# Kernel tuning notes

Measured on AMD Instinct MI355X. Metric: run time of the kernel, lower is better.

## Reference

```python
import jax, jax.numpy as jnp
import numpy as np

SCALE = 1.0 / np.sqrt(512.0).astype(np.float32)  # attention() hardcodes d_k=512


def setup_inputs() -> dict:
    key = jax.random.key(0)
    ks = jax.random.split(key, 9)
    B, S, D = 4, 2048, 512
    mk = lambda k, shape: jax.random.normal(k, shape, dtype=jnp.float32) * 0.05
    return {
        "q": mk(ks[0], (B, S, D)),
        "k": mk(ks[1], (B, S, D)),
        "v": mk(ks[2], (B, S, D)),
        "WQ_w": mk(ks[3], (D, D)),
        "WQ_b": mk(ks[4], (D,)),
        "WK_w": mk(ks[5], (D, D)),
        "WK_b": mk(ks[6], (D,)),
        "WV_w": mk(ks[7], (D, D)),
        "WV_b": mk(ks[8], (D,)),
    }


def reference(q, k, v, WQ_w, WQ_b, WK_w, WK_b, WV_w, WV_b):
    # torch nn.Linear: y = x @ W.T + b
    qp = q @ WQ_w.T + WQ_b  # [B,S,dk]
    kp = k @ WK_w.T + WK_b  # [B,S,dk]
    vp = v @ WV_w.T + WV_b  # [B,S,dv]
    qk = jnp.einsum("bqd,bkd->bqk", qp, kp) * SCALE  # [B,Sq,Sk]
    S = qk.shape[1]
    tril = jnp.tril(jnp.ones((S, S), dtype=qk.dtype))  # multiplicative causal mask
    qk = qk * tril
    # NOTE: original applies softmax over dim=1 (the query axis), faithfully kept.
    attn = jax.nn.softmax(qk, axis=1)
    out = jnp.einsum("bqk,bkd->bqd", attn, vp)  # [B,Sq,dv]
    return out
```

## Files before the change

kernel.cpp:

```cpp
#include <hip/hip_runtime.h>
#include <hip/hip_bf16.h>


#define S_LEN 2048
#define D_DIM 512
#define SCALE_F 0.044194173824159216f

typedef __attribute__((ext_vector_type(8))) short s8v;
typedef __attribute__((ext_vector_type(4))) short s4v;
typedef __attribute__((ext_vector_type(4))) float f4v;

enum { EPI_BIAS = 0, EPI_BIAS_T = 1, EPI_SCORES = 2 };

#define SBAR()    __builtin_amdgcn_s_barrier()
#define SCHEDB()  __builtin_amdgcn_sched_barrier(0)
#define WAITV(n)  asm volatile("s_waitcnt vmcnt(" #n ")")
#define WAITL0()  asm volatile("s_waitcnt lgkmcnt(0)")

__device__ __forceinline__ short f2bf_s(float f) {
  union { __hip_bfloat16 b; short s; } u; u.b = __float2bfloat16(f); return u.s;
}
__device__ __forceinline__ float bf2f_s(short h) {
  union { short s; __hip_bfloat16 b; } u; u.s = h; return __bfloat162float(u.b);
}

__device__ __forceinline__ void glds16(const short* g, short* l) {
  __builtin_amdgcn_global_load_lds((const __attribute__((address_space(1))) void*)g,
                                   (__attribute__((address_space(3))) void*)l, 16, 0, 0);
}

__device__ __forceinline__ unsigned lds_addr(const short* p) {
  return (unsigned)(unsigned long long)(const __attribute__((address_space(3))) short*)p;
}

__device__ __forceinline__ s8v dsr128(unsigned a) {
  s8v r;
  asm volatile("ds_read_b128 %0, %1" : "=&v"(r) : "v"(a));
  return r;
}

template <int EPI>
__device__ __forceinline__ void gemm_core(
    const short* __restrict__ A, const short* __restrict__ B,
    short* __restrict__ C, const float* __restrict__ bias,
    short* SMEM, int N, int K, size_t sCz, int m0, int n0, int bz,
    float* __restrict__ Z)
{
  const int tid  = threadIdx.x;
  const int w    = tid >> 6;
  const int lane = tid & 63;
  const int quad = lane >> 4;
  const int l16  = lane & 15;
  const int wm   = (w >> 1) * 64;
  const int wn   = (w & 1) * 64;

  const int strow = tid >> 3;
  const int gl = ((tid & 7) ^ (strow & 7)) * 8;

  f4v acc[4][4];
#pragma unroll
  for (int i = 0; i < 4; ++i)
#pragma unroll
    for (int j = 0; j < 4; ++j)
#pragma unroll
      for (int r = 0; r < 4; ++r) acc[i][j][r] = 0.0f;

  const short* Ag = A + (size_t)(m0 + strow) * K + gl;
  const short* Bg = B + (size_t)(n0 + strow) * K + gl;
  const size_t pstr = (size_t)32 * K;
  const int t8 = tid * 8;
  const int swq = l16 & 7;

  const unsigned base = lds_addr(SMEM);
  unsigned aoff[4], boff[4];
#pragma unroll
  for (int ii = 0; ii < 4; ++ii)
    aoff[ii] = base + (unsigned)((wm + ii * 16 + l16) * 128 + ((quad ^ swq) * 16));
#pragma unroll
  for (int j = 0; j < 4; ++j)
    boff[j] = base + 16384u + (unsigned)((wn + j * 16 + l16) * 128 + ((quad ^ swq) * 16));

  const int niter = K >> 6;

#pragma unroll
  for (int p = 0; p < 4; ++p) glds16(Ag + p * pstr, SMEM + t8 + p * 2048);
#pragma unroll
  for (int p = 0; p < 4; ++p) glds16(Bg + p * pstr, SMEM + 8192 + t8 + p * 2048);

  for (int i = 0; i < niter; ++i) {
    const int c = i & 1;
    if (i + 1 < niter) {
      const int k1 = (i + 1) << 6;
      short* dA = SMEM + (1 - c) * 16384 + t8;
#pragma unroll
      for (int p = 0; p < 4; ++p) glds16(Ag + k1 + p * pstr, dA + p * 2048);
#pragma unroll
      for (int p = 0; p < 4; ++p) glds16(Bg + k1 + p * pstr, dA + 8192 + p * 2048);
      SCHEDB();
      WAITV(8);
    } else {
      WAITV(0);
    }
    SBAR();
    SCHEDB();

    const unsigned cofs = (unsigned)(c << 15);
#pragma unroll
    for (int kk = 0; kk < 2; ++kk) {
      const unsigned kx = (unsigned)(kk << 6);
      s8v af[4], bf[4];
#pragma unroll
      for (int ii = 0; ii < 4; ++ii) af[ii] = dsr128((aoff[ii] ^ kx) + cofs);
#pragma unroll
      for (int j = 0; j < 4; ++j)   bf[j]  = dsr128((boff[j] ^ kx) + cofs);
      WAITL0();
      SCHEDB();
      __builtin_amdgcn_s_setprio(1);
#pragma unroll
      for (int ii = 0; ii < 4; ++ii)
#pragma unroll
        for (int j = 0; j < 4; ++j)
          acc[ii][j] = __builtin_amdgcn_mfma_f32_16x16x32_bf16(af[ii], bf[j], acc[ii][j], 0, 0, 0);
      __builtin_amdgcn_s_setprio(0);
    }
    SBAR();
  }

  float bv[4];
  if (EPI == EPI_BIAS || EPI == EPI_BIAS_T) {
#pragma unroll
    for (int j = 0; j < 4; ++j) bv[j] = bias[n0 + wn + j * 16 + l16];
  }

  if (EPI == EPI_BIAS_T) {
#pragma unroll
    for (int i = 0; i < 4; ++i) {
#pragma unroll
      for (int j = 0; j < 4; ++j) {
        const int gn  = n0 + wn + j * 16 + l16;
        const int gmb = m0 + wm + i * 16 + quad * 4;
        const int bb = gmb >> 11, ssb = gmb & (S_LEN - 1);
        s4v o;
#pragma unroll
        for (int r = 0; r < 4; ++r) o[r] = f2bf_s(acc[i][j][r] + bv[j]);
        *(s4v*)&C[((size_t)bb * D_DIM + gn) * S_LEN + ssb] = o;
      }
    }
    return;
  }

  short* TB = SMEM;
  const int wbase = w * 2176;
  float csum[4] = {0.f, 0.f, 0.f, 0.f};

#pragma unroll
  for (int ph = 0; ph < 2; ++ph) {
    __syncthreads();
#pragma unroll
    for (int ii = 0; ii < 2; ++ii) {
      const int i = ph * 2 + ii;
#pragma unroll
      for (int j = 0; j < 4; ++j) {
        const int gn = n0 + wn + j * 16 + l16;
#pragma unroll
        for (int r = 0; r < 4; ++r) {
          short o;
          if (EPI == EPI_SCORES) {
            const int gm = m0 + wm + i * 16 + quad * 4 + r;
            const float f = (gm >= gn) ? (__expf(acc[i][j][r] * SCALE_F) - 1.0f) : 0.0f;
            csum[j] += f;
            o = f2bf_s(f);
          } else {
            o = f2bf_s(acc[i][j][r] + bv[j]);
          }
          TB[wbase + (ii * 16 + quad * 4 + r) * 68 + j * 16 + l16] = o;
        }
      }
    }
    __syncthreads();
#pragma unroll
    for (int p = 0; p < 4; ++p) {
      const int row = p * 8 + (lane >> 3);
      const int cg  = lane & 7;
      const s8v vv = *(const s8v*)&TB[wbase + row * 68 + cg * 8];
      const int gm = m0 + wm + ph * 32 + row;
      const int gn = n0 + wn + cg * 8;
      *(s8v*)&C[sCz + (size_t)gm * N + gn] = vv;
    }
  }

  if (EPI == EPI_SCORES) {
#pragma unroll
    for (int j = 0; j < 4; ++j) {
      float cs = csum[j];
      cs += __shfl_xor(cs, 16, 64);
      cs += __shfl_xor(cs, 32, 64);
      if (quad == 0) atomicAdd(&Z[(bz << 11) + n0 + wn + j * 16 + l16], cs);
    }
  }
}

__global__ __launch_bounds__(256, 2) void proj_qk(
    const short* __restrict__ a0, const short* __restrict__ a1,
    const short* __restrict__ b0, const short* __restrict__ b1,
    short* __restrict__ c0, short* __restrict__ c1,
    const float* __restrict__ x0, const float* __restrict__ x1)
{
  __shared__ __align__(16) short SMEM[32768];
  const int bid = blockIdx.x;
  const int bsw = (bid & 7) * 64 + (bid >> 3);
  const int z   = bsw >> 8;
  const int rem = bsw & 255;
  const int m0  = (rem >> 2) * 128;
  const int n0  = (rem & 3) * 128;
  const short* A = z ? a1 : a0;
  const short* B = z ? b1 : b0;
  short*       C = z ? c1 : c0;
  const float* bias = z ? x1 : x0;
  gemm_core<EPI_BIAS>(A, B, C, bias, SMEM, D_DIM, D_DIM, 0, m0, n0, 0, nullptr);
}

__global__ __launch_bounds__(256, 2) void scores_projv(
    const short* __restrict__ qp, const short* __restrict__ kp, short* __restrict__ F,
    float* __restrict__ Z,
    const short* __restrict__ vb, const short* __restrict__ Wvb,
    short* __restrict__ vpT, const float* __restrict__ xv)
{
  __shared__ __align__(16) short SMEM[32768];
  const int bid = blockIdx.x;
  if (bid < 544) {
    const int bsw = (bid & 7) * 68 + (bid >> 3);
    const int bz  = bsw / 136;
    const int t   = bsw - bz * 136;
    int ti = (int)((sqrtf(8.0f * t + 1.0f) - 1.0f) * 0.5f);
    while ((ti + 1) * (ti + 2) / 2 <= t) ++ti;
    while (ti * (ti + 1) / 2 > t) --ti;
    const int tj = t - ti * (ti + 1) / 2;
    gemm_core<EPI_SCORES>(qp + (size_t)bz * S_LEN * D_DIM, kp + (size_t)bz * S_LEN * D_DIM,
                          F, nullptr, SMEM, S_LEN, D_DIM,
                          (size_t)bz * S_LEN * S_LEN, ti * 128, tj * 128, bz, Z);
  } else {
    const int h   = bid - 544;
    const int hsw = (h & 7) * 32 + (h >> 3);
    const int m0  = (hsw >> 2) * 128;
    const int n0  = (hsw & 3) * 128;
    gemm_core<EPI_BIAS_T>(vb, Wvb, vpT, xv, SMEM, D_DIM, D_DIM, 0, m0, n0, 0, nullptr);
  }
}

__global__ __launch_bounds__(256, 2) void gemm_outF(
    const short* __restrict__ F, const short* __restrict__ vpT,
    const float* __restrict__ Tv, float* __restrict__ out)
{
  __shared__ __align__(16) short SMEM[36864];

  const int tid  = threadIdx.x;
  const int h    = blockIdx.x;
  const int n0   = (h & 3) * 128;
  const int bz   = (h >> 2) & 3;
  const int zs   = h >> 4;
  const int mi   = (zs < 16) ? (31 - zs) : (zs - 16);
  const int m0   = mi * 64;

  const short* A = F   + (size_t)bz * S_LEN * S_LEN;
  const short* B = vpT + (size_t)bz * D_DIM * S_LEN;

  const int w    = tid >> 6;
  const int lane = tid & 63;
  const int quad = lane >> 4;
  const int l16  = lane & 15;
  const int wm   = (w >> 1) * 32;
  const int wn   = (w & 1) * 64;

  const int strow = tid >> 3;
  const int gl = ((tid & 7) ^ (strow & 7)) * 8;

  f4v acc[2][4];
#pragma unroll
  for (int i = 0; i < 2; ++i)
#pragma unroll
    for (int j = 0; j < 4; ++j)
#pragma unroll
      for (int r = 0; r < 4; ++r) acc[i][j][r] = 0.0f;

  const short* Ag = A + (size_t)(m0 + strow) * S_LEN + gl;
  const short* Bg = B + (size_t)(n0 + strow) * S_LEN + gl;
  const size_t pstr = (size_t)32 * S_LEN;
  const int t8 = tid * 8;
  const int swq = l16 & 7;

  const unsigned base = lds_addr(SMEM);
  unsigned aoff[2], boff[4];
#pragma unroll
  for (int ii = 0; ii < 2; ++ii)
    aoff[ii] = base + (unsigned)((wm + ii * 16 + l16) * 128 + ((quad ^ swq) * 16));
#pragma unroll
  for (int j = 0; j < 4; ++j)
    boff[j] = base + 8192u + (unsigned)((wn + j * 16 + l16) * 128 + ((quad ^ swq) * 16));

  const int niter = mi + 1;

#pragma unroll
  for (int pre = 0; pre < 2; ++pre) {
    short* dst = SMEM + pre * 12288 + t8;
    const int k0 = pre << 6;
#pragma unroll
    for (int p = 0; p < 2; ++p) glds16(Ag + k0 + p * pstr, dst + p * 2048);
#pragma unroll
    for (int p = 0; p < 4; ++p) glds16(Bg + k0 + p * pstr, dst + 4096 + p * 2048);
  }

  int cbuf = 0;
  for (int i = 0; i < niter; ++i) {
    if (i + 1 < niter) { WAITV(6); } else { WAITV(0); }
    SBAR();
    SCHEDB();

    if (i + 2 < niter) {
      int nb = cbuf + 2; if (nb >= 3) nb -= 3;
      const int k2 = (i + 2) << 6;
      short* dst = SMEM + nb * 12288 + t8;
#pragma unroll
      for (int p = 0; p < 2; ++p) glds16(Ag + k2 + p * pstr, dst + p * 2048);
#pragma unroll
      for (int p = 0; p < 4; ++p) glds16(Bg + k2 + p * pstr, dst + 4096 + p * 2048);
      SCHEDB();
    }

    const unsigned cofs = (unsigned)(cbuf * 24576);
    cbuf = (cbuf == 2) ? 0 : cbuf + 1;
#pragma unroll
    for (int kk = 0; kk < 2; ++kk) {
      const unsigned kx = (unsigned)(kk << 6);
      s8v af[2], bf[4];
#pragma unroll
      for (int ii = 0; ii < 2; ++ii) af[ii] = dsr128((aoff[ii] ^ kx) + cofs);
#pragma unroll
      for (int j = 0; j < 4; ++j)   bf[j]  = dsr128((boff[j] ^ kx) + cofs);
      WAITL0();
      SCHEDB();
      __builtin_amdgcn_s_setprio(1);
#pragma unroll
      for (int ii = 0; ii < 2; ++ii)
#pragma unroll
        for (int j = 0; j < 4; ++j)
          acc[ii][j] = __builtin_amdgcn_mfma_f32_16x16x32_bf16(af[ii], bf[j], acc[ii][j], 0, 0, 0);
      __builtin_amdgcn_s_setprio(0);
    }
  }

  float* Cf = out + (size_t)bz * S_LEN * D_DIM;
#pragma unroll
  for (int i = 0; i < 2; ++i) {
#pragma unroll
    for (int j = 0; j < 4; ++j) {
      const int gn = n0 + wn + j * 16 + l16;
      const float tvn = Tv[(bz << 9) + gn];
#pragma unroll
      for (int r = 0; r < 4; ++r) {
        const int gm = m0 + wm + i * 16 + quad * 4 + r;
        Cf[(size_t)gm * D_DIM + gn] = acc[i][j][r] + tvn;
      }
    }
  }
}

__global__ __launch_bounds__(256) void cvt_all(
    const float* __restrict__ q, const float* __restrict__ k, const float* __restrict__ v,
    const float* __restrict__ wq, const float* __restrict__ wk, const float* __restrict__ wv,
    short* __restrict__ qb, short* __restrict__ kb, short* __restrict__ vb,
    short* __restrict__ Wqb, short* __restrict__ Wkb, short* __restrict__ Wvb,
    float* __restrict__ ZF)
{
  const int y = blockIdx.y;
  const float* s; short* d; int i;
  if (blockIdx.x < 2048) {
    s = (y == 0) ? q : (y == 1) ? k : v;
    d = (y == 0) ? qb : (y == 1) ? kb : vb;
    i = (blockIdx.x * 256 + threadIdx.x) * 8;
    if (y == 0) {
      const int gid = blockIdx.x * 256 + threadIdx.x;
      if (gid < 8192) ZF[gid] = 0.0f;
    }
  } else {
    s = (y == 0) ? wq : (y == 1) ? wk : wv;
    d = (y == 0) ? Wqb : (y == 1) ? Wkb : Wvb;
    i = ((int)(blockIdx.x - 2048) * 256 + threadIdx.x) * 8;
  }
  const float4 f0 = *(const float4*)(s + i);
  const float4 f1 = *(const float4*)(s + i + 4);
  s8v o;
  o[0] = f2bf_s(f0.x); o[1] = f2bf_s(f0.y); o[2] = f2bf_s(f0.z); o[3] = f2bf_s(f0.w);
  o[4] = f2bf_s(f1.x); o[5] = f2bf_s(f1.y); o[6] = f2bf_s(f1.z); o[7] = f2bf_s(f1.w);
  *(s8v*)(d + i) = o;
}

__global__ __launch_bounds__(256) void scale_vpt_T(
    short* __restrict__ vpT, const float* __restrict__ ZF, float* __restrict__ Tv)
{
  __shared__ float red[4];
  const int b = blockIdx.y, d = blockIdx.x, tid = threadIdx.x;
  const size_t rowbase = ((size_t)(b * D_DIM + d)) * S_LEN;
  const float* zf = ZF + (b << 11);
  const int k0 = tid * 8;

  s8v v = *(s8v*)&vpT[rowbase + k0];
  float s = 0.0f;
#pragma unroll
  for (int i = 0; i < 8; ++i) {
    const float w = bf2f_s(v[i]) / (2048.0f + zf[k0 + i]);
    s += w;
    v[i] = f2bf_s(w);
  }
  *(s8v*)&vpT[rowbase + k0] = v;

#pragma unroll
  for (int off = 32; off >= 1; off >>= 1) s += __shfl_xor(s, off, 64);
  if ((tid & 63) == 0) red[tid >> 6] = s;
  __syncthreads();
  if (tid == 0) Tv[(b << 9) + d] = red[0] + red[1] + red[2] + red[3];
}

extern "C" void kernel_launch(void* const* d_in, const int* in_sizes, int n_in,
                              void* d_out, int out_size, void* d_ws, size_t ws_size,
                              hipStream_t stream) {
  const float* q   = (const float*)d_in[0];
  const float* k   = (const float*)d_in[1];
  const float* v   = (const float*)d_in[2];
  const float* WQw = (const float*)d_in[3];
  const float* WQb = (const float*)d_in[4];
  const float* WKw = (const float*)d_in[5];
  const float* WKb = (const float*)d_in[6];
  const float* WVw = (const float*)d_in[7];
  const float* WVb = (const float*)d_in[8];

  char* ws = (char*)d_ws;
  short* F   = (short*)(ws);
  short* qb  = (short*)(ws);
  short* kb  = qb + 4194304;
  short* Wqb = (short*)(ws + 25165824);
  short* Wkb = Wqb + 262144;
  short* qp  = (short*)(ws + 33554432);
  short* kp  = (short*)(ws + 41943040);
  short* vpT = (short*)(ws + 50331648);
  float* ZF  = (float*)(ws + 58720256);
  float* Tv  = (float*)(ws + 58753024);
  short* vb  = (short*)d_out;
  short* Wvb = (short*)d_out + 4194304;

  const dim3 blk(256);

  cvt_all<<<dim3(2176, 3), blk, 0, stream>>>(
      q, k, v, WQw, WKw, WVw, qb, kb, vb, Wqb, Wkb, Wvb, ZF);

  proj_qk<<<dim3(512), blk, 0, stream>>>(qb, kb, Wqb, Wkb, qp, kp, WQb, WKb);

  scores_projv<<<dim3(800), blk, 0, stream>>>(qp, kp, F, ZF, vb, Wvb, vpT, WVb);

  scale_vpt_T<<<dim3(512, 4), blk, 0, stream>>>(vpT, ZF, Tv);

  gemm_outF<<<dim3(512), blk, 0, stream>>>(F, vpT, Tv, (float*)d_out);
}
```

Measured before the change: 164.4 us.

## Use 256x256 GEMM tiles with 512 threads and fold V projection into projection kernel

Replaces the 128x128, 256-thread GEMM core with a 256x256, 512-thread core that stages 64-wide K slices into 128KB of dynamic LDS. Each wave now computes a 128x64 sub-tile, with B fragments reused across four A phases. The Q, K and V projections run in one 192-block launch, and the causal score GEMM uses 144 triangular 256x256 tiles. The aim is more operand reuse per LDS load and fewer launches and blocks, at the cost of far fewer blocks than CUs, one block per CU because of the LDS size, and more wasted work on diagonal tiles.

```diff
diff --git a/kernel.cpp b/kernel.cpp
--- a/kernel.cpp
+++ b/kernel.cpp
@@ -40,62 +40,61 @@
 }
 
 template <int EPI>
-__device__ __forceinline__ void gemm_core(
+__device__ __forceinline__ void gemm256_core(
     const short* __restrict__ A, const short* __restrict__ B,
     short* __restrict__ C, const float* __restrict__ bias,
-    short* SMEM, int N, int K, size_t sCz, int m0, int n0, int bz,
-    float* __restrict__ Z)
+    short* SMEM, int N, size_t sCz, int m0, int n0, float* __restrict__ Z)
 {
   const int tid  = threadIdx.x;
   const int w    = tid >> 6;
   const int lane = tid & 63;
   const int quad = lane >> 4;
   const int l16  = lane & 15;
-  const int wm   = (w >> 1) * 64;
-  const int wn   = (w & 1) * 64;
+  const int wr   = w >> 2;
+  const int wc   = w & 3;
 
   const int strow = tid >> 3;
   const int gl = ((tid & 7) ^ (strow & 7)) * 8;
-
-  f4v acc[4][4];
-#pragma unroll
-  for (int i = 0; i < 4; ++i)
-#pragma unroll
-    for (int j = 0; j < 4; ++j)
-#pragma unroll
-      for (int r = 0; r < 4; ++r) acc[i][j][r] = 0.0f;
-
-  const short* Ag = A + (size_t)(m0 + strow) * K + gl;
-  const short* Bg = B + (size_t)(n0 + strow) * K + gl;
-  const size_t pstr = (size_t)32 * K;
   const int t8 = tid * 8;
   const int swq = l16 & 7;
 
+  f4v acc[8][4];
+#pragma unroll
+  for (int i = 0; i < 8; ++i)
+#pragma unroll
+    for (int j = 0; j < 4; ++j)
+#pragma unroll
+      for (int r = 0; r < 4; ++r) acc[i][j][r] = 0.0f;
+
+  const short* Ag = A + (size_t)(m0 + strow) * 512 + gl;
+  const short* Bg = B + (size_t)(n0 + strow) * 512 + gl;
+  const size_t pstr = (size_t)64 * 512;
+
   const unsigned base = lds_addr(SMEM);
-  unsigned aoff[4], boff[4];
-#pragma unroll
-  for (int ii = 0; ii < 4; ++ii)
-    aoff[ii] = base + (unsigned)((wm + ii * 16 + l16) * 128 + ((quad ^ swq) * 16));
-#pragma unroll
-  for (int j = 0; j < 4; ++j)
-    boff[j] = base + 16384u + (unsigned)((wn + j * 16 + l16) * 128 + ((quad ^ swq) * 16));
-
-  const int niter = K >> 6;
-
-#pragma unroll
-  for (int p = 0; p < 4; ++p) glds16(Ag + p * pstr, SMEM + t8 + p * 2048);
-#pragma unroll
-  for (int p = 0; p < 4; ++p) glds16(Bg + p * pstr, SMEM + 8192 + t8 + p * 2048);
-
-  for (int i = 0; i < niter; ++i) {
-    const int c = i & 1;
-    if (i + 1 < niter) {
-      const int k1 = (i + 1) << 6;
-      short* dA = SMEM + (1 - c) * 16384 + t8;
-#pragma unroll
-      for (int p = 0; p < 4; ++p) glds16(Ag + k1 + p * pstr, dA + p * 2048);
-#pragma unroll
-      for (int p = 0; p < 4; ++p) glds16(Bg + k1 + p * pstr, dA + 8192 + p * 2048);
+  unsigned aoff[8], boff[4];
+#pragma unroll
+  for (int mf = 0; mf < 8; ++mf)
+    aoff[mf] = base + (unsigned)((wr * 128 + mf * 16 + l16) * 128 + ((quad ^ swq) * 16));
+#pragma unroll
+  for (int nf = 0; nf < 4; ++nf)
+    boff[nf] = base + 32768u + (unsigned)((wc * 64 + nf * 16 + l16) * 128 + ((quad ^ swq) * 16));
+
+#define STG256(kt, b)                                                          \
+  {                                                                            \
+    short* dst_ = SMEM + (b) * 32768 + t8;                                     \
+    const int ko_ = (kt) << 6;                                                 \
+    _Pragma("unroll")                                                          \
+    for (int p = 0; p < 4; ++p) glds16(Ag + ko_ + p * pstr, dst_ + p * 4096);  \
+    _Pragma("unroll")                                                          \
+    for (int p = 0; p < 4; ++p) glds16(Bg + ko_ + p * pstr, dst_ + 16384 + p * 4096); \
+  }
+
+  STG256(0, 0);
+
+  for (int t = 0; t < 8; ++t) {
+    const int c = t & 1;
+    if (t < 7) {
+      STG256(t + 1, 1 - c);
       SCHEDB();
       WAITV(8);
     } else {
@@ -104,45 +103,58 @@
     SBAR();
     SCHEDB();
 
-    const unsigned cofs = (unsigned)(c << 15);
-#pragma unroll
-    for (int kk = 0; kk < 2; ++kk) {
-      const unsigned kx = (unsigned)(kk << 6);
-      s8v af[4], bf[4];
-#pragma unroll
-      for (int ii = 0; ii < 4; ++ii) af[ii] = dsr128((aoff[ii] ^ kx) + cofs);
-#pragma unroll
-      for (int j = 0; j < 4; ++j)   bf[j]  = dsr128((boff[j] ^ kx) + cofs);
+    const unsigned cofs = (unsigned)(c << 16);
+
+    s8v bf[2][4];
+#pragma unroll
+    for (int kk = 0; kk < 2; ++kk)
+#pragma unroll
+      for (int nf = 0; nf < 4; ++nf)
+        bf[kk][nf] = dsr128((boff[nf] ^ (unsigned)(kk << 6)) + cofs);
+
+#pragma unroll
+    for (int ph = 0; ph < 4; ++ph) {
+      s8v af[2][2];
+#pragma unroll
+      for (int mi = 0; mi < 2; ++mi)
+#pragma unroll
+        for (int kk = 0; kk < 2; ++kk)
+          af[mi][kk] = dsr128((aoff[ph * 2 + mi] ^ (unsigned)(kk << 6)) + cofs);
       WAITL0();
       SCHEDB();
       __builtin_amdgcn_s_setprio(1);
 #pragma unroll
-      for (int ii = 0; ii < 4; ++ii)
-#pragma unroll
-        for (int j = 0; j < 4; ++j)
-          acc[ii][j] = __builtin_amdgcn_mfma_f32_16x16x32_bf16(af[ii], bf[j], acc[ii][j], 0, 0, 0);
+      for (int mi = 0; mi < 2; ++mi)
+#pragma unroll
+        for (int kk = 0; kk < 2; ++kk)
+#pragma unroll
+          for (int nf = 0; nf < 4; ++nf)
+            acc[ph * 2 + mi][nf] =
+                __builtin_amdgcn_mfma_f32_16x16x32_bf16(af[mi][kk], bf[kk][nf],
+                                                        acc[ph * 2 + mi][nf], 0, 0, 0);
       __builtin_amdgcn_s_setprio(0);
-    }
-    SBAR();
-  }
+      SBAR();
+    }
+  }
+#undef STG256
 
   float bv[4];
   if (EPI == EPI_BIAS || EPI == EPI_BIAS_T) {
 #pragma unroll
-    for (int j = 0; j < 4; ++j) bv[j] = bias[n0 + wn + j * 16 + l16];
+    for (int nf = 0; nf < 4; ++nf) bv[nf] = bias[n0 + wc * 64 + nf * 16 + l16];
   }
 
   if (EPI == EPI_BIAS_T) {
 #pragma unroll
-    for (int i = 0; i < 4; ++i) {
-#pragma unroll
-      for (int j = 0; j < 4; ++j) {
-        const int gn  = n0 + wn + j * 16 + l16;
-        const int gmb = m0 + wm + i * 16 + quad * 4;
+    for (int mf = 0; mf < 8; ++mf) {
+#pragma unroll
+      for (int nf = 0; nf < 4; ++nf) {
+        const int gn  = n0 + wc * 64 + nf * 16 + l16;
+        const int gmb = m0 + wr * 128 + mf * 16 + quad * 4;
         const int bb = gmb >> 11, ssb = gmb & (S_LEN - 1);
         s4v o;
 #pragma unroll
-        for (int r = 0; r < 4; ++r) o[r] = f2bf_s(acc[i][j][r] + bv[j]);
+        for (int r = 0; r < 4; ++r) o[r] = f2bf_s(acc[mf][nf][r] + bv[nf]);
         *(s4v*)&C[((size_t)bb * D_DIM + gn) * S_LEN + ssb] = o;
       }
     }
@@ -154,26 +166,26 @@
   float csum[4] = {0.f, 0.f, 0.f, 0.f};
 
 #pragma unroll
-  for (int ph = 0; ph < 2; ++ph) {
+  for (int ph = 0; ph < 4; ++ph) {
     __syncthreads();
 #pragma unroll
     for (int ii = 0; ii < 2; ++ii) {
-      const int i = ph * 2 + ii;
-#pragma unroll
-      for (int j = 0; j < 4; ++j) {
-        const int gn = n0 + wn + j * 16 + l16;
+      const int mf = ph * 2 + ii;
+#pragma unroll
+      for (int nf = 0; nf < 4; ++nf) {
+        const int gn = n0 + wc * 64 + nf * 16 + l16;
 #pragma unroll
         for (int r = 0; r < 4; ++r) {
           short o;
           if (EPI == EPI_SCORES) {
-            const int gm = m0 + wm + i * 16 + quad * 4 + r;
-            const float f = (gm >= gn) ? (__expf(acc[i][j][r] * SCALE_F) - 1.0f) : 0.0f;
-            csum[j] += f;
+            const int gm = m0 + wr * 128 + mf * 16 + quad * 4 + r;
+            const float f = (gm >= gn) ? (__expf(acc[mf][nf][r] * SCALE_F) - 1.0f) : 0.0f;
+            csum[nf] += f;
             o = f2bf_s(f);
           } else {
-            o = f2bf_s(acc[i][j][r] + bv[j]);
+            o = f2bf_s(acc[mf][nf][r] + bv[nf]);
           }
-          TB[wbase + (ii * 16 + quad * 4 + r) * 68 + j * 16 + l16] = o;
+          TB[wbase + (ii * 16 + quad * 4 + r) * 68 + nf * 16 + l16] = o;
         }
       }
     }
@@ -183,69 +195,63 @@
       const int row = p * 8 + (lane >> 3);
       const int cg  = lane & 7;
       const s8v vv = *(const s8v*)&TB[wbase + row * 68 + cg * 8];
-      const int gm = m0 + wm + ph * 32 + row;
-      const int gn = n0 + wn + cg * 8;
+      const int gm = m0 + wr * 128 + ph * 32 + row;
+      const int gn = n0 + wc * 64 + cg * 8;
       *(s8v*)&C[sCz + (size_t)gm * N + gn] = vv;
     }
   }
 
   if (EPI == EPI_SCORES) {
 #pragma unroll
-    for (int j = 0; j < 4; ++j) {
-      float cs = csum[j];
+    for (int nf = 0; nf < 4; ++nf) {
+      float cs = csum[nf];
       cs += __shfl_xor(cs, 16, 64);
       cs += __shfl_xor(cs, 32, 64);
-      if (quad == 0) atomicAdd(&Z[(bz << 11) + n0 + wn + j * 16 + l16], cs);
-    }
-  }
-}
-
-__global__ __launch_bounds__(256, 2) void proj_qk(
-    const short* __restrict__ a0, const short* __restrict__ a1,
-    const short* __restrict__ b0, const short* __restrict__ b1,
-    short* __restrict__ c0, short* __restrict__ c1,
-    const float* __restrict__ x0, const float* __restrict__ x1)
-{
-  __shared__ __align__(16) short SMEM[32768];
+      if (quad == 0) atomicAdd(&Z[n0 + wc * 64 + nf * 16 + l16], cs);
+    }
+  }
+}
+
+__global__ __launch_bounds__(512, 2) void proj256(
+    const short* __restrict__ qb, const short* __restrict__ kb, const short* __restrict__ vb,
+    const short* __restrict__ Wqb, const short* __restrict__ Wkb, const short* __restrict__ Wvb,
+    short* __restrict__ qp, short* __restrict__ kp, short* __restrict__ vpT,
+    const float* __restrict__ xq, const float* __restrict__ xk, const float* __restrict__ xv)
+{
+  extern __shared__ short SMEM[];
   const int bid = blockIdx.x;
-  const int bsw = (bid & 7) * 64 + (bid >> 3);
-  const int z   = bsw >> 8;
-  const int rem = bsw & 255;
-  const int m0  = (rem >> 2) * 128;
-  const int n0  = (rem & 3) * 128;
-  const short* A = z ? a1 : a0;
-  const short* B = z ? b1 : b0;
-  short*       C = z ? c1 : c0;
-  const float* bias = z ? x1 : x0;
-  gemm_core<EPI_BIAS>(A, B, C, bias, SMEM, D_DIM, D_DIM, 0, m0, n0, 0, nullptr);
-}
-
-__global__ __launch_bounds__(256, 2) void scores_projv(
+  const int bsw = (bid & 7) * 24 + (bid >> 3);
+  const int z   = bsw >> 6;
+  const int rem = bsw & 63;
+  const int m0  = (rem >> 1) * 256;
+  const int n0  = (rem & 1) * 256;
+  const short* A = (z == 0) ? qb : (z == 1) ? kb : vb;
+  const short* B = (z == 0) ? Wqb : (z == 1) ? Wkb : Wvb;
+  short*       C = (z == 0) ? qp : (z == 1) ? kp : vpT;
+  const float* bias = (z == 0) ? xq : (z == 1) ? xk : xv;
+  if (z == 2)
+    gemm256_core<EPI_BIAS_T>(A, B, C, bias, SMEM, D_DIM, 0, m0, n0, nullptr);
+  else
+    gemm256_core<EPI_BIAS>(A, B, C, bias, SMEM, D_DIM, 0, m0, n0, nullptr);
+}
+
+__global__ __launch_bounds__(512, 2) void scores256(
     const short* __restrict__ qp, const short* __restrict__ kp, short* __restrict__ F,
-    float* __restrict__ Z,
-    const short* __restrict__ vb, const short* __restrict__ Wvb,
-    short* __restrict__ vpT, const float* __restrict__ xv)
-{
-  __shared__ __align__(16) short SMEM[32768];
+    float* __restrict__ Z)
+{
+  extern __shared__ short SMEM[];
   const int bid = blockIdx.x;
-  if (bid < 544) {
-    const int bsw = (bid & 7) * 68 + (bid >> 3);
-    const int bz  = bsw / 136;
-    const int t   = bsw - bz * 136;
-    int ti = (int)((sqrtf(8.0f * t + 1.0f) - 1.0f) * 0.5f);
-    while ((ti + 1) * (ti + 2) / 2 <= t) ++ti;
-    while (ti * (ti + 1) / 2 > t) --ti;
-    const int tj = t - ti * (ti + 1) / 2;
-    gemm_core<EPI_SCORES>(qp + (size_t)bz * S_LEN * D_DIM, kp + (size_t)bz * S_LEN * D_DIM,
-                          F, nullptr, SMEM, S_LEN, D_DIM,
-                          (size_t)bz * S_LEN * S_LEN, ti * 128, tj * 128, bz, Z);
-  } else {
-    const int h   = bid - 544;
-    const int hsw = (h & 7) * 32 + (h >> 3);
-    const int m0  = (hsw >> 2) * 128;
-    const int n0  = (hsw & 3) * 128;
-    gemm_core<EPI_BIAS_T>(vb, Wvb, vpT, xv, SMEM, D_DIM, D_DIM, 0, m0, n0, 0, nullptr);
-  }
+  const int bsw = (bid & 7) * 18 + (bid >> 3);
+  const int bz  = bsw / 36;
+  const int t   = bsw - bz * 36;
+  int ti = (int)((sqrtf(8.0f * t + 1.0f) - 1.0f) * 0.5f);
+  while ((ti + 1) * (ti + 2) / 2 <= t) ++ti;
+  while (ti * (ti + 1) / 2 > t) --ti;
+  const int tj = t - ti * (ti + 1) / 2;
+  gemm256_core<EPI_SCORES>(qp + (size_t)bz * S_LEN * D_DIM, kp + (size_t)bz * S_LEN * D_DIM,
+                           F, nullptr, SMEM, S_LEN,
+                           (size_t)bz * S_LEN * S_LEN, ti * 256, tj * 256,
+                           Z + (bz << 11));
 }
 
 __global__ __launch_bounds__(256, 2) void gemm_outF(
@@ -438,24 +444,34 @@
   short* F   = (short*)(ws);
   short* qb  = (short*)(ws);
   short* kb  = qb + 4194304;
+  short* vb  = qb + 8388608;
   short* Wqb = (short*)(ws + 25165824);
   short* Wkb = Wqb + 262144;
+  short* Wvb = Wqb + 524288;
   short* qp  = (short*)(ws + 33554432);
   short* kp  = (short*)(ws + 41943040);
   short* vpT = (short*)(ws + 50331648);
   float* ZF  = (float*)(ws + 58720256);
   float* Tv  = (float*)(ws + 58753024);
-  short* vb  = (short*)d_out;
-  short* Wvb = (short*)d_out + 4194304;
+
+  static bool attr_done = false;
+  if (!attr_done) {
+    (void)hipFuncSetAttribute((const void*)proj256,
+                              hipFuncAttributeMaxDynamicSharedMemorySize, 131072);
+    (void)hipFuncSetAttribute((const void*)scores256,
+                              hipFuncAttributeMaxDynamicSharedMemorySize, 131072);
+    attr_done = true;
+  }
 
   const dim3 blk(256);
 
   cvt_all<<<dim3(2176, 3), blk, 0, stream>>>(
       q, k, v, WQw, WKw, WVw, qb, kb, vb, Wqb, Wkb, Wvb, ZF);
 
-  proj_qk<<<dim3(512), blk, 0, stream>>>(qb, kb, Wqb, Wkb, qp, kp, WQb, WKb);
-
-  scores_projv<<<dim3(800), blk, 0, stream>>>(qp, kp, F, ZF, vb, Wvb, vpT, WVb);
+  proj256<<<dim3(192), dim3(512), 131072, stream>>>(
+      qb, kb, vb, Wqb, Wkb, Wvb, qp, kp, vpT, WQb, WKb, WVb);
+
+  scores256<<<dim3(144), dim3(512), 131072, stream>>>(qp, kp, F, ZF);
 
   scale_vpt_T<<<dim3(512, 4), blk, 0, stream>>>(vpT, ZF, Tv);
 
```

Result: slower. 179.8 us (+9.4%).

## Fuse all five stages into one persistent kernel with grid barriers

Applied to the files above, without the earlier changes.

Merges the conversion, QK projection, scores/V-projection, V scaling and output GEMM launches into a single persistent 512-block kernel. Stages are separated by a hierarchical atomic grid barrier, and a memset resets the barrier counters each call. The output GEMM also drops from a three-stage to a double-buffered LDS pipeline with an extra barrier per iteration, so it fits in the smaller shared buffer. This removes launch gaps and tail effects, at the cost of barrier overhead, load imbalance within each stage, and a reliance on all 512 blocks being resident at once to avoid deadlock.

```diff
diff --git a/kernel.cpp b/kernel.cpp
--- a/kernel.cpp
+++ b/kernel.cpp
@@ -37,6 +37,34 @@
   s8v r;
   asm volatile("ds_read_b128 %0, %1" : "=&v"(r) : "v"(a));
   return r;
+}
+
+__device__ __forceinline__ void gsync(int* bars, int phase) {
+  __syncthreads();
+  if (threadIdx.x == 0) {
+    const int g = (int)(blockIdx.x & 7);
+    int* cnt = bars + g * 64;
+    int* rel = bars + g * 64 + 32;
+    __threadfence();
+    const int a = __hip_atomic_fetch_add(cnt, 1, __ATOMIC_RELAXED, __HIP_MEMORY_SCOPE_AGENT);
+    if (a == phase * 64 + 63) {
+      int* root = bars + 512;
+      const int r = __hip_atomic_fetch_add(root, 1, __ATOMIC_RELAXED, __HIP_MEMORY_SCOPE_AGENT);
+      if (r == phase * 8 + 7) {
+#pragma unroll
+        for (int x = 0; x < 8; ++x)
+          __hip_atomic_store(bars + x * 64 + 32, phase + 1,
+                             __ATOMIC_RELAXED, __HIP_MEMORY_SCOPE_AGENT);
+      }
+    }
+    int guard = 0;
+    while (__hip_atomic_load(rel, __ATOMIC_RELAXED, __HIP_MEMORY_SCOPE_AGENT) <= phase) {
+      __builtin_amdgcn_s_sleep(2);
+      if (++guard > (1 << 20)) break;
+    }
+    __threadfence();
+  }
+  __syncthreads();
 }
 
 template <int EPI>
@@ -200,66 +228,12 @@
   }
 }
 
-__global__ __launch_bounds__(256, 2) void proj_qk(
-    const short* __restrict__ a0, const short* __restrict__ a1,
-    const short* __restrict__ b0, const short* __restrict__ b1,
-    short* __restrict__ c0, short* __restrict__ c1,
-    const float* __restrict__ x0, const float* __restrict__ x1)
+__device__ __forceinline__ void outF_body(
+    const short* __restrict__ F, const short* __restrict__ vpT,
+    const float* __restrict__ Tv, float* __restrict__ out,
+    int bz, int mi, int n0, short* SMEM)
 {
-  __shared__ __align__(16) short SMEM[32768];
-  const int bid = blockIdx.x;
-  const int bsw = (bid & 7) * 64 + (bid >> 3);
-  const int z   = bsw >> 8;
-  const int rem = bsw & 255;
-  const int m0  = (rem >> 2) * 128;
-  const int n0  = (rem & 3) * 128;
-  const short* A = z ? a1 : a0;
-  const short* B = z ? b1 : b0;
-  short*       C = z ? c1 : c0;
-  const float* bias = z ? x1 : x0;
-  gemm_core<EPI_BIAS>(A, B, C, bias, SMEM, D_DIM, D_DIM, 0, m0, n0, 0, nullptr);
-}
-
-__global__ __launch_bounds__(256, 2) void scores_projv(
-    const short* __restrict__ qp, const short* __restrict__ kp, short* __restrict__ F,
-    float* __restrict__ Z,
-    const short* __restrict__ vb, const short* __restrict__ Wvb,
-    short* __restrict__ vpT, const float* __restrict__ xv)
-{
-  __shared__ __align__(16) short SMEM[32768];
-  const int bid = blockIdx.x;
-  if (bid < 544) {
-    const int bsw = (bid & 7) * 68 + (bid >> 3);
-    const int bz  = bsw / 136;
-    const int t   = bsw - bz * 136;
-    int ti = (int)((sqrtf(8.0f * t + 1.0f) - 1.0f) * 0.5f);
-    while ((ti + 1) * (ti + 2) / 2 <= t) ++ti;
-    while (ti * (ti + 1) / 2 > t) --ti;
-    const int tj = t - ti * (ti + 1) / 2;
-    gemm_core<EPI_SCORES>(qp + (size_t)bz * S_LEN * D_DIM, kp + (size_t)bz * S_LEN * D_DIM,
-                          F, nullptr, SMEM, S_LEN, D_DIM,
-                          (size_t)bz * S_LEN * S_LEN, ti * 128, tj * 128, bz, Z);
-  } else {
-    const int h   = bid - 544;
-    const int hsw = (h & 7) * 32 + (h >> 3);
-    const int m0  = (hsw >> 2) * 128;
-    const int n0  = (hsw & 3) * 128;
-    gemm_core<EPI_BIAS_T>(vb, Wvb, vpT, xv, SMEM, D_DIM, D_DIM, 0, m0, n0, 0, nullptr);
-  }
-}
-
-__global__ __launch_bounds__(256, 2) void gemm_outF(
-    const short* __restrict__ F, const short* __restrict__ vpT,
-    const float* __restrict__ Tv, float* __restrict__ out)
-{
-  __shared__ __align__(16) short SMEM[36864];
-
   const int tid  = threadIdx.x;
-  const int h    = blockIdx.x;
-  const int n0   = (h & 3) * 128;
-  const int bz   = (h >> 2) & 3;
-  const int zs   = h >> 4;
-  const int mi   = (zs < 16) ? (31 - zs) : (zs - 16);
   const int m0   = mi * 64;
 
   const short* A = F   + (size_t)bz * S_LEN * S_LEN;
@@ -301,34 +275,28 @@
   const int niter = mi + 1;
 
 #pragma unroll
-  for (int pre = 0; pre < 2; ++pre) {
-    short* dst = SMEM + pre * 12288 + t8;
-    const int k0 = pre << 6;
-#pragma unroll
-    for (int p = 0; p < 2; ++p) glds16(Ag + k0 + p * pstr, dst + p * 2048);
-#pragma unroll
-    for (int p = 0; p < 4; ++p) glds16(Bg + k0 + p * pstr, dst + 4096 + p * 2048);
-  }
-
-  int cbuf = 0;
+  for (int p = 0; p < 2; ++p) glds16(Ag + p * pstr, SMEM + t8 + p * 2048);
+#pragma unroll
+  for (int p = 0; p < 4; ++p) glds16(Bg + p * pstr, SMEM + 4096 + t8 + p * 2048);
+
   for (int i = 0; i < niter; ++i) {
-    if (i + 1 < niter) { WAITV(6); } else { WAITV(0); }
+    const int c = i & 1;
+    if (i + 1 < niter) {
+      const int k1 = (i + 1) << 6;
+      short* dst = SMEM + (1 - c) * 12288 + t8;
+#pragma unroll
+      for (int p = 0; p < 2; ++p) glds16(Ag + k1 + p * pstr, dst + p * 2048);
+#pragma unroll
+      for (int p = 0; p < 4; ++p) glds16(Bg + k1 + p * pstr, dst + 4096 + p * 2048);
+      SCHEDB();
+      WAITV(6);
+    } else {
+      WAITV(0);
+    }
     SBAR();
     SCHEDB();
 
-    if (i + 2 < niter) {
-      int nb = cbuf + 2; if (nb >= 3) nb -= 3;
-      const int k2 = (i + 2) << 6;
-      short* dst = SMEM + nb * 12288 + t8;
-#pragma unroll
-      for (int p = 0; p < 2; ++p) glds16(Ag + k2 + p * pstr, dst + p * 2048);
-#pragma unroll
-      for (int p = 0; p < 4; ++p) glds16(Bg + k2 + p * pstr, dst + 4096 + p * 2048);
-      SCHEDB();
-    }
-
-    const unsigned cofs = (unsigned)(cbuf * 24576);
-    cbuf = (cbuf == 2) ? 0 : cbuf + 1;
+    const unsigned cofs = (unsigned)(c * 24576);
 #pragma unroll
     for (int kk = 0; kk < 2; ++kk) {
       const unsigned kx = (unsigned)(kk << 6);
@@ -347,6 +315,7 @@
           acc[ii][j] = __builtin_amdgcn_mfma_f32_16x16x32_bf16(af[ii], bf[j], acc[ii][j], 0, 0, 0);
       __builtin_amdgcn_s_setprio(0);
     }
+    SBAR();
   }
 
   float* Cf = out + (size_t)bz * S_LEN * D_DIM;
@@ -365,60 +334,139 @@
   }
 }
 
-__global__ __launch_bounds__(256) void cvt_all(
+__global__ __launch_bounds__(256, 2) void fused_pipeline(
     const float* __restrict__ q, const float* __restrict__ k, const float* __restrict__ v,
-    const float* __restrict__ wq, const float* __restrict__ wk, const float* __restrict__ wv,
-    short* __restrict__ qb, short* __restrict__ kb, short* __restrict__ vb,
-    short* __restrict__ Wqb, short* __restrict__ Wkb, short* __restrict__ Wvb,
-    float* __restrict__ ZF)
+    const float* __restrict__ WQw, const float* __restrict__ WQb,
+    const float* __restrict__ WKw, const float* __restrict__ WKb,
+    const float* __restrict__ WVw, const float* __restrict__ WVb,
+    char* __restrict__ ws, float* __restrict__ out, int* __restrict__ bars)
 {
-  const int y = blockIdx.y;
-  const float* s; short* d; int i;
-  if (blockIdx.x < 2048) {
-    s = (y == 0) ? q : (y == 1) ? k : v;
-    d = (y == 0) ? qb : (y == 1) ? kb : vb;
-    i = (blockIdx.x * 256 + threadIdx.x) * 8;
-    if (y == 0) {
-      const int gid = blockIdx.x * 256 + threadIdx.x;
-      if (gid < 8192) ZF[gid] = 0.0f;
-    }
-  } else {
-    s = (y == 0) ? wq : (y == 1) ? wk : wv;
-    d = (y == 0) ? Wqb : (y == 1) ? Wkb : Wvb;
-    i = ((int)(blockIdx.x - 2048) * 256 + threadIdx.x) * 8;
-  }
-  const float4 f0 = *(const float4*)(s + i);
-  const float4 f1 = *(const float4*)(s + i + 4);
-  s8v o;
-  o[0] = f2bf_s(f0.x); o[1] = f2bf_s(f0.y); o[2] = f2bf_s(f0.z); o[3] = f2bf_s(f0.w);
-  o[4] = f2bf_s(f1.x); o[5] = f2bf_s(f1.y); o[6] = f2bf_s(f1.z); o[7] = f2bf_s(f1.w);
-  *(s8v*)(d + i) = o;
-}
-
-__global__ __launch_bounds__(256) void scale_vpt_T(
-    short* __restrict__ vpT, const float* __restrict__ ZF, float* __restrict__ Tv)
-{
-  __shared__ float red[4];
-  const int b = blockIdx.y, d = blockIdx.x, tid = threadIdx.x;
-  const size_t rowbase = ((size_t)(b * D_DIM + d)) * S_LEN;
-  const float* zf = ZF + (b << 11);
-  const int k0 = tid * 8;
-
-  s8v v = *(s8v*)&vpT[rowbase + k0];
-  float s = 0.0f;
-#pragma unroll
-  for (int i = 0; i < 8; ++i) {
-    const float w = bf2f_s(v[i]) / (2048.0f + zf[k0 + i]);
-    s += w;
-    v[i] = f2bf_s(w);
-  }
-  *(s8v*)&vpT[rowbase + k0] = v;
-
-#pragma unroll
-  for (int off = 32; off >= 1; off >>= 1) s += __shfl_xor(s, off, 64);
-  if ((tid & 63) == 0) red[tid >> 6] = s;
-  __syncthreads();
-  if (tid == 0) Tv[(b << 9) + d] = red[0] + red[1] + red[2] + red[3];
+  __shared__ __align__(16) short SMEM[32768];
+  const int bid = blockIdx.x;
+  const int tid = threadIdx.x;
+  const int tg  = bid * 256 + tid;
+
+  short* F   = (short*)(ws);
+  short* qb  = (short*)(ws);
+  short* kb  = qb + 4194304;
+  short* Wqb = (short*)(ws + 25165824);
+  short* Wkb = Wqb + 262144;
+  short* qp  = (short*)(ws + 33554432);
+  short* kp  = (short*)(ws + 41943040);
+  short* vpT = (short*)(ws + 50331648);
+  float* ZF  = (float*)(ws + 58720256);
+  float* Tv  = (float*)(ws + 58753024);
+  short* vb  = (short*)out;
+  short* Wvb = (short*)out + 4194304;
+
+  {
+#pragma unroll 2
+    for (int sw = 0; sw < 12; ++sw) {
+      const int e = (sw * 131072 + tg) * 8;
+      const float* s; short* d; int off;
+      if (e < 4194304)       { s = q; d = qb; off = e; }
+      else if (e < 8388608)  { s = k; d = kb; off = e - 4194304; }
+      else                   { s = v; d = vb; off = e - 8388608; }
+      const float4 f0 = *(const float4*)(s + off);
+      const float4 f1 = *(const float4*)(s + off + 4);
+      s8v o;
+      o[0] = f2bf_s(f0.x); o[1] = f2bf_s(f0.y); o[2] = f2bf_s(f0.z); o[3] = f2bf_s(f0.w);
+      o[4] = f2bf_s(f1.x); o[5] = f2bf_s(f1.y); o[6] = f2bf_s(f1.z); o[7] = f2bf_s(f1.w);
+      *(s8v*)(d + off) = o;
+    }
+    if (tg < 98304) {
+      const int e = tg * 8;
+      const float* s; short* d; int off;
+      if (e < 262144)        { s = WQw; d = Wqb; off = e; }
+      else if (e < 524288)   { s = WKw; d = Wkb; off = e - 262144; }
+      else                   { s = WVw; d = Wvb; off = e - 524288; }
+      const float4 f0 = *(const float4*)(s + off);
+      const float4 f1 = *(const float4*)(s + off + 4);
+      s8v o;
+      o[0] = f2bf_s(f0.x); o[1] = f2bf_s(f0.y); o[2] = f2bf_s(f0.z); o[3] = f2bf_s(f0.w);
+      o[4] = f2bf_s(f1.x); o[5] = f2bf_s(f1.y); o[6] = f2bf_s(f1.z); o[7] = f2bf_s(f1.w);
+      *(s8v*)(d + off) = o;
+    }
+    if (tg < 8192) ZF[tg] = 0.0f;
+  }
+  gsync(bars, 0);
+
+  {
+    const int bsw = (bid & 7) * 64 + (bid >> 3);
+    const int z   = bsw >> 8;
+    const int rem = bsw & 255;
+    const int m0  = (rem >> 2) * 128;
+    const int n0  = (rem & 3) * 128;
+    const short* A = z ? kb : qb;
+    const short* B = z ? Wkb : Wqb;
+    short*       C = z ? kp : qp;
+    const float* bias = z ? WKb : WQb;
+    gemm_core<EPI_BIAS>(A, B, C, bias, SMEM, D_DIM, D_DIM, 0, m0, n0, 0, nullptr);
+  }
+  gsync(bars, 1);
+
+  for (int rep = 0; rep < 2; ++rep) {
+    const int t = bid + rep * 512;
+    if (t >= 800) break;
+    if (t < 544) {
+      const int bsw = (t & 7) * 68 + (t >> 3);
+      const int bz  = bsw / 136;
+      const int tt  = bsw - bz * 136;
+      int ti = (int)((sqrtf(8.0f * tt + 1.0f) - 1.0f) * 0.5f);
+      while ((ti + 1) * (ti + 2) / 2 <= tt) ++ti;
+      while (ti * (ti + 1) / 2 > tt) --ti;
+      const int tj = tt - ti * (ti + 1) / 2;
+      gemm_core<EPI_SCORES>(qp + (size_t)bz * S_LEN * D_DIM, kp + (size_t)bz * S_LEN * D_DIM,
+                            F, nullptr, SMEM, S_LEN, D_DIM,
+                            (size_t)bz * S_LEN * S_LEN, ti * 128, tj * 128, bz, ZF);
+    } else {
+      const int h   = t - 544;
+      const int hsw = (h & 7) * 32 + (h >> 3);
+      const int m0  = (hsw >> 2) * 128;
+      const int n0  = (hsw & 3) * 128;
+      gemm_core<EPI_BIAS_T>(vb, Wvb, vpT, WVb, SMEM, D_DIM, D_DIM, 0, m0, n0, 0, nullptr);
+    }
+  }
+  gsync(bars, 2);
+
+  {
+    float* red = (float*)SMEM;
+#pragma unroll
+    for (int it = 0; it < 4; ++it) {
+      const int r = bid + 512 * it;
+      const int b = r >> 9, d = r & 511;
+      const size_t rowbase = ((size_t)(b * D_DIM + d)) * S_LEN;
+      const float* zf = ZF + (b << 11);
+      const int k0 = tid * 8;
+      s8v vv = *(s8v*)&vpT[rowbase + k0];
+      float s = 0.0f;
+#pragma unroll
+      for (int i = 0; i < 8; ++i) {
+        const float wgt = bf2f_s(vv[i]) / (2048.0f + zf[k0 + i]);
+        s += wgt;
+        vv[i] = f2bf_s(wgt);
+      }
+      *(s8v*)&vpT[rowbase + k0] = vv;
+#pragma unroll
+      for (int off = 32; off >= 1; off >>= 1) s += __shfl_xor(s, off, 64);
+      if ((tid & 63) == 0) red[tid >> 6] = s;
+      __syncthreads();
+      if (tid == 0) Tv[(b << 9) + d] = red[0] + red[1] + red[2] + red[3];
+      __syncthreads();
+    }
+  }
+  gsync(bars, 3);
+
+  {
+    const int x     = bid & 7;
+    const int s     = bid >> 3;
+    const int n0    = (s & 3) * 128;
+    const int bz    = (s >> 2) & 3;
+    const int zslot = s >> 4;
+    const int zs    = (zslot < 2) ? (2 * x + zslot) : (16 + 2 * x + (zslot - 2));
+    const int mi    = (zs < 16) ? (31 - zs) : (zs - 16);
+    outF_body(F, vpT, Tv, out, bz, mi, n0, SMEM);
+  }
 }
 
 extern "C" void kernel_launch(void* const* d_in, const int* in_sizes, int n_in,
@@ -435,29 +483,11 @@
   const float* WVb = (const float*)d_in[8];
 
   char* ws = (char*)d_ws;
-  short* F   = (short*)(ws);
-  short* qb  = (short*)(ws);
-  short* kb  = qb + 4194304;
-  short* Wqb = (short*)(ws + 25165824);
-  short* Wkb = Wqb + 262144;
-  short* qp  = (short*)(ws + 33554432);
-  short* kp  = (short*)(ws + 41943040);
-  short* vpT = (short*)(ws + 50331648);
-  float* ZF  = (float*)(ws + 58720256);
-  float* Tv  = (float*)(ws + 58753024);
-  short* vb  = (short*)d_out;
-  short* Wvb = (short*)d_out + 4194304;
-
-  const dim3 blk(256);
-
-  cvt_all<<<dim3(2176, 3), blk, 0, stream>>>(
-      q, k, v, WQw, WKw, WVw, qb, kb, vb, Wqb, Wkb, Wvb, ZF);
-
-  proj_qk<<<dim3(512), blk, 0, stream>>>(qb, kb, Wqb, Wkb, qp, kp, WQb, WKb);
-
-  scores_projv<<<dim3(800), blk, 0, stream>>>(qp, kp, F, ZF, vb, Wvb, vpT, WVb);
-
-  scale_vpt_T<<<dim3(512, 4), blk, 0, stream>>>(vpT, ZF, Tv);
-
-  gemm_outF<<<dim3(512), blk, 0, stream>>>(F, vpT, Tv, (float*)d_out);
-}
+  int* bars = (int*)(ws + 58761216);
+
+  (void)hipMemsetAsync(bars, 0, 4096, stream);
+
+  fused_pipeline<<<dim3(512), dim3(256), 0, stream>>>(
+      q, k, v, WQw, WQb, WKw, WKb, WVw, WVb,
+      ws, (float*)d_out, bars);
+}
```

Measured after the change: 257.0 us. 56.3% more time.
